# Optimization experiments

Measured on AMD Instinct MI355X. Metric: run time of the kernel, lower is better.

The kernel has to match this reference:

```python
import jax, jax.numpy as jnp
import numpy as np

TAU = 2.0      # LIF membrane time constant (spikingjelly LIFNode tau=2.0)
V_TH = 1.0     # default spikingjelly threshold
ALPHA = 2.0    # ATan surrogate default alpha

@jax.custom_vjp
def atan_spike(x):
    # Heaviside forward, ATan surrogate backward (spikingjelly surrogate.ATan)
    return (x >= 0.0).astype(x.dtype)

def _spike_fwd(x):
    return atan_spike(x), x

def _spike_bwd(x, g):
    sg = (ALPHA / 2.0) / (1.0 + (jnp.pi / 2.0 * ALPHA * x) ** 2)
    return (g * sg,)

atan_spike.defvjp(_spike_fwd, _spike_bwd)


def setup_inputs() -> dict:
    key = jax.random.key(0)
    ks = jax.random.split(key, 4)
    B, L, C, H, NL, K = 64, 96, 32, 256, 2, 3
    inputs = jax.random.normal(ks[0], (B, L, C), jnp.float32)
    w_enc = jax.random.normal(ks[1], (H, 1, K), jnp.float32) * (1.0 / np.sqrt(K))
    b_enc = jnp.zeros((H,), jnp.float32)
    w_rnn = jax.random.normal(ks[2], (NL, H, H), jnp.float32) * (1.0 / np.sqrt(H))
    b_rnn = jnp.zeros((NL, H), jnp.float32)
    return {"inputs": inputs, "w_enc": w_enc, "b_enc": b_enc,
            "w_rnn": w_rnn, "b_rnn": b_rnn}


def reference(inputs, w_enc, b_enc, w_rnn, b_rnn):
    B, L, C = inputs.shape
    H = w_enc.shape[0]
    NL = w_rnn.shape[0]
    # --- 'conv' spike encoder: per-channel temporal conv -> [B*C, H, L] ---
    x = inputs.transpose(0, 2, 1).reshape(B * C, 1, L)
    h = jax.lax.conv_general_dilated(x, w_enc, (1,), 'SAME',
                                     dimension_numbers=('NCH', 'OIH', 'NCH'))
    h = h + b_enc[None, :, None]
    h = h.transpose(2, 0, 1)  # [L, B*C, H] time-major for scan

    def step(v, x_t):
        s = x_t
        new_v = []
        for l in range(NL):  # fixed small layer loop
            cur = s @ w_rnn[l].T + b_rnn[l]            # Linear
            vl = v[l] + (cur - v[l]) / TAU             # leaky integrate
            s = atan_spike(vl - V_TH)                  # fire (surrogate grad)
            vl = vl * (1.0 - jax.lax.stop_gradient(s)) # hard reset, detach_reset
            new_v.append(vl)
        return tuple(new_v), (s, new_v[-1])

    v0 = tuple(jnp.zeros((B * C, H), inputs.dtype) for _ in range(NL))
    _, (spks, mems) = jax.lax.scan(step, v0, h)
    # spks: [L, B*C, H] -> [B, C*H, L]
    spks = spks.reshape(L, B, C * H).transpose(1, 2, 0)
    return spks.transpose(0, 2, 1), spks[:, :, -1]
```

## Files before the change

kernel.cpp:

```cpp
#include <hip/hip_runtime.h>
#include <hip/hip_bf16.h>
#include <stdint.h>


using floatx4 = __attribute__((ext_vector_type(4))) float;
using intx4   = __attribute__((ext_vector_type(4))) int;

__global__ void prep_kernel(const float* __restrict__ w_enc,
                            const float* __restrict__ b_enc,
                            const float* __restrict__ w_rnn,
                            const float* __restrict__ b_rnn,
                            double* __restrict__ Wd,
                            double* __restrict__ C0d,
                            signed char* __restrict__ Bw8)
{
    const int o = blockIdx.x;
    const int lane = threadIdx.x;
    const float4 w0v = *(const float4*)(w_rnn + (size_t)o * 256 + lane * 4);
    double a0 = 0.0, a1 = 0.0, a2 = 0.0, ab = 0.0;
#pragma unroll
    for (int e = 0; e < 4; ++e) {
        const int i = lane * 4 + e;
        const double wv = (double)(((const float*)&w0v)[e]);
        a0 += wv * (double)w_enc[i * 3 + 0];
        a1 += wv * (double)w_enc[i * 3 + 1];
        a2 += wv * (double)w_enc[i * 3 + 2];
        ab += wv * (double)b_enc[i];
    }
    for (int off = 32; off > 0; off >>= 1) {
        a0 += __shfl_down(a0, off, 64);
        a1 += __shfl_down(a1, off, 64);
        a2 += __shfl_down(a2, off, 64);
        ab += __shfl_down(ab, off, 64);
    }
    if (lane == 0) {
        Wd[o * 3 + 0] = a0;
        Wd[o * 3 + 1] = a1;
        Wd[o * 3 + 2] = a2;
        C0d[o] = ab + (double)b_rnn[o];
    }
    const float4 w1v = *(const float4*)(w_rnn + 65536 + (size_t)o * 256 + lane * 4);
    unsigned int pack[4] = {0u, 0u, 0u, 0u};
#pragma unroll
    for (int e = 0; e < 4; ++e) {
        float f = ((const float*)&w1v)[e];
        int q = __double2int_rn((double)f * 134217728.0);
        int d3 = ((q + 64) & 127) - 64;  q = (q - d3) >> 7;
        int d2 = ((q + 64) & 127) - 64;  q = (q - d2) >> 7;
        int d1 = ((q + 64) & 127) - 64;  q = (q - d1) >> 7;
        int d0 = q;
        pack[0] |= ((unsigned int)(d0 & 0xFF)) << (8 * e);
        pack[1] |= ((unsigned int)(d1 & 0xFF)) << (8 * e);
        pack[2] |= ((unsigned int)(d2 & 0xFF)) << (8 * e);
        pack[3] |= ((unsigned int)(d3 & 0xFF)) << (8 * e);
    }
#pragma unroll
    for (int l = 0; l < 4; ++l)
        *(unsigned int*)(Bw8 + ((size_t)o * 4 + l) * 256 + lane * 4) = pack[l];
}

__global__ void enc_kernel(const float* __restrict__ inputs,
                           const double* __restrict__ Wd,
                           const double* __restrict__ C0d,
                           unsigned char* __restrict__ s0b)
{
    const int n = blockIdx.x;
    const int tidx = threadIdx.x;
    const int b = n >> 5, c = n & 31;
    __shared__ float xr[98];
    if (tidx < 96)       xr[tidx + 1] = inputs[((size_t)b * 96 + tidx) * 32 + c];
    else if (tidx == 96) xr[0]  = 0.0f;
    else if (tidx == 97) xr[97] = 0.0f;
    __syncthreads();
    const double W0 = Wd[tidx * 3], W1 = Wd[tidx * 3 + 1], W2 = Wd[tidx * 3 + 2];
    const double c0 = C0d[tidx];
    const int wid = tidx >> 6, lane = tidx & 63;
    float v = 0.0f;
    for (int t = 0; t < 96; ++t) {
        float cur = (float)((double)xr[t] * W0 + (double)xr[t + 1] * W1 +
                            (double)xr[t + 2] * W2 + c0);
        float vv = v + (cur - v) * 0.5f;
        int sp = (vv - 1.0f) >= 0.0f;
        v = sp ? 0.0f : vv;
        unsigned long long bal = __ballot(sp);
        if ((lane & 15) == 0) {
            const int j = lane >> 4;
            *(unsigned short*)(s0b + ((size_t)t * 2048 + n) * 32 + 8 * j + 2 * wid)
                = (unsigned short)(bal >> (16 * j));
        }
    }
}

__global__ __launch_bounds__(256, 2) void rnn_kernel(
    const unsigned char* __restrict__ s0b,
    const signed char* __restrict__ Bw8,
    const float* __restrict__ b_rnn,
    float* __restrict__ out0,
    float* __restrict__ out1)
{
    const int tid  = threadIdx.x;
    const int wid  = tid >> 6, lane = tid & 63;
    const int m    = lane & 15, g = lane >> 4;
    const int job  = blockIdx.x * 4 + wid;
    const int rt   = job >> 4;
    const int nw   = rt * 16;
    const int o0   = (job & 15) * 16;

    intx4 bfrag[4][4];
#pragma unroll
    for (int l = 0; l < 4; ++l)
#pragma unroll
        for (int c = 0; c < 4; ++c)
            bfrag[l][c] = *(const intx4*)(Bw8 + ((size_t)(o0 + m) * 4 + l) * 256
                                               + c * 64 + g * 16);
    const float4 biasv = *(const float4*)(b_rnn + 256 + o0 + g * 4);

    float* pb = out0 + ((size_t)(nw >> 5) * 96) * 8192
                     + (size_t)((nw & 31) + m) * 256 + o0 + g * 4;

    const unsigned char* mp = s0b + ((size_t)(nw + m)) * 32 + 8 * g;
    uint2 m0 = *(const uint2*)(mp);
    uint2 m1 = *(const uint2*)(mp + 65536);

    floatx4 v = {0.f, 0.f, 0.f, 0.f};

    #define STEP_MFMA(MASK, ACC0, ACC1, ACC2, ACC3)                            \
    do {                                                                       \
        unsigned int hw_[4] = { (MASK).x & 0xFFFFu, (MASK).x >> 16,            \
                                (MASK).y & 0xFFFFu, (MASK).y >> 16 };          \
        _Pragma("unroll")                                                      \
        for (int c = 0; c < 4; ++c) {                                          \
            unsigned int h_ = hw_[c];                                          \
            intx4 a_;                                                          \
            a_.x = (int)((( h_        & 0xFu) * 0x00204081u) & 0x01010101u);   \
            a_.y = (int)((((h_ >> 4)  & 0xFu) * 0x00204081u) & 0x01010101u);   \
            a_.z = (int)((((h_ >> 8)  & 0xFu) * 0x00204081u) & 0x01010101u);   \
            a_.w = (int)((((h_ >> 12) & 0xFu) * 0x00204081u) & 0x01010101u);   \
            ACC0 = __builtin_amdgcn_mfma_i32_16x16x64_i8(bfrag[0][c], a_, ACC0, 0, 0, 0); \
            ACC1 = __builtin_amdgcn_mfma_i32_16x16x64_i8(bfrag[1][c], a_, ACC1, 0, 0, 0); \
            ACC2 = __builtin_amdgcn_mfma_i32_16x16x64_i8(bfrag[2][c], a_, ACC2, 0, 0, 0); \
            ACC3 = __builtin_amdgcn_mfma_i32_16x16x64_i8(bfrag[3][c], a_, ACC3, 0, 0, 0); \
        }                                                                      \
    } while (0)

    for (int t = 0; t < 95; ++t) {
        uint2 nxt = m1;
        m1 = *(const uint2*)(mp + (size_t)(t + 2) * 65536);

        intx4 acc0 = {0,0,0,0}, acc1 = {0,0,0,0}, acc2 = {0,0,0,0}, acc3 = {0,0,0,0};
        STEP_MFMA(m0, acc0, acc1, acc2, acc3);

        float4 sv;
#pragma unroll
        for (int r = 0; r < 4; ++r) {
            int a01 = acc0[r] * 128 + acc1[r];
            int a23 = acc2[r] * 128 + acc3[r];
            float cur = fmaf((float)a01, 0x1p-13f, (float)a23 * 0x1p-27f)
                        + ((const float*)&biasv)[r];
            float vv = v[r];
            vv = vv + (cur - vv) * 0.5f;
            float s = ((vv - 1.0f) >= 0.0f) ? 1.0f : 0.0f;
            v[r] = vv * (1.0f - s);
            ((float*)&sv)[r] = s;
        }
        *(float4*)pb = sv;
        pb += 8192;
        m0 = nxt;
    }

    {
        intx4 acc0 = {0,0,0,0}, acc1 = {0,0,0,0}, acc2 = {0,0,0,0}, acc3 = {0,0,0,0};
        STEP_MFMA(m0, acc0, acc1, acc2, acc3);
        float4 sv;
#pragma unroll
        for (int r = 0; r < 4; ++r) {
            int a01 = acc0[r] * 128 + acc1[r];
            int a23 = acc2[r] * 128 + acc3[r];
            float cur = fmaf((float)a01, 0x1p-13f, (float)a23 * 0x1p-27f)
                        + ((const float*)&biasv)[r];
            float vv = v[r];
            vv = vv + (cur - vv) * 0.5f;
            float s = ((vv - 1.0f) >= 0.0f) ? 1.0f : 0.0f;
            ((float*)&sv)[r] = s;
        }
        *(float4*)pb = sv;
        *(float4*)(out1 + (size_t)(nw + m) * 256 + o0 + g * 4) = sv;
    }
    #undef STEP_MFMA
}

extern "C" void kernel_launch(void* const* d_in, const int* in_sizes, int n_in,
                              void* d_out, int out_size, void* d_ws, size_t ws_size,
                              hipStream_t stream) {
    const float* inputs = (const float*)d_in[0];
    const float* w_enc  = (const float*)d_in[1];
    const float* b_enc  = (const float*)d_in[2];
    const float* w_rnn  = (const float*)d_in[3];
    const float* b_rnn  = (const float*)d_in[4];

    float* out0 = (float*)d_out;
    float* out1 = out0 + (size_t)64 * 96 * 8192;

    char* ws = (char*)d_ws;
    double*      Wd  = (double*)(ws);
    double*      C0d = (double*)(ws + 6144);
    signed char* Bw8 = (signed char*)(ws + 8192);
    unsigned char* s0b = (unsigned char*)(ws + 270336);

    prep_kernel<<<256, 64, 0, stream>>>(w_enc, b_enc, w_rnn, b_rnn, Wd, C0d, Bw8);
    enc_kernel<<<2048, 256, 0, stream>>>(inputs, Wd, C0d, s0b);
    rnn_kernel<<<512, 256, 0, stream>>>(s0b, Bw8, b_rnn, out0, out1);
}
```

Measured before the change: 257.9 us.

## Store layer-0 spikes as bytes to skip bitmask expansion in RNN kernel

The encoder now writes each layer-0 spike as a full byte instead of a ballot-packed bitmask. The RNN kernel then loads the bytes directly as int8 MFMA A-fragments, removing the per-step multiply-and-mask bit expansion. The cost is an 8x larger intermediate buffer (about 48 MB instead of 6 MB), which raises global memory write and read traffic and uses more workspace. The spike/reset select is also rewritten from multiply form to select form.

```diff
diff --git a/kernel.cpp b/kernel.cpp
--- a/kernel.cpp
+++ b/kernel.cpp
@@ -62,7 +62,7 @@
 __global__ void enc_kernel(const float* __restrict__ inputs,
                            const double* __restrict__ Wd,
                            const double* __restrict__ C0d,
-                           unsigned char* __restrict__ s0b)
+                           unsigned char* __restrict__ s0B)
 {
     const int n = blockIdx.x;
     const int tidx = threadIdx.x;
@@ -74,7 +74,7 @@
     __syncthreads();
     const double W0 = Wd[tidx * 3], W1 = Wd[tidx * 3 + 1], W2 = Wd[tidx * 3 + 2];
     const double c0 = C0d[tidx];
-    const int wid = tidx >> 6, lane = tidx & 63;
+    unsigned char* po = s0B + (size_t)n * 256 + tidx;
     float v = 0.0f;
     for (int t = 0; t < 96; ++t) {
         float cur = (float)((double)xr[t] * W0 + (double)xr[t + 1] * W1 +
@@ -82,17 +82,12 @@
         float vv = v + (cur - v) * 0.5f;
         int sp = (vv - 1.0f) >= 0.0f;
         v = sp ? 0.0f : vv;
-        unsigned long long bal = __ballot(sp);
-        if ((lane & 15) == 0) {
-            const int j = lane >> 4;
-            *(unsigned short*)(s0b + ((size_t)t * 2048 + n) * 32 + 8 * j + 2 * wid)
-                = (unsigned short)(bal >> (16 * j));
-        }
+        po[(size_t)t * 524288] = (unsigned char)sp;
     }
 }
 
 __global__ __launch_bounds__(256, 2) void rnn_kernel(
-    const unsigned char* __restrict__ s0b,
+    const unsigned char* __restrict__ s0B,
     const signed char* __restrict__ Bw8,
     const float* __restrict__ b_rnn,
     float* __restrict__ out0,
@@ -118,37 +113,45 @@
     float* pb = out0 + ((size_t)(nw >> 5) * 96) * 8192
                      + (size_t)((nw & 31) + m) * 256 + o0 + g * 4;
 
-    const unsigned char* mp = s0b + ((size_t)(nw + m)) * 32 + 8 * g;
-    uint2 m0 = *(const uint2*)(mp);
-    uint2 m1 = *(const uint2*)(mp + 65536);
+    const unsigned char* sp_base = s0B + (size_t)(nw + m) * 256 + 16 * g;
+    uint4 cb0 = *(const uint4*)(sp_base);
+    uint4 cb1 = *(const uint4*)(sp_base + 64);
+    uint4 cb2 = *(const uint4*)(sp_base + 128);
+    uint4 cb3 = *(const uint4*)(sp_base + 192);
 
     floatx4 v = {0.f, 0.f, 0.f, 0.f};
 
-    #define STEP_MFMA(MASK, ACC0, ACC1, ACC2, ACC3)                            \
+    #define STEP_MFMA(B0, B1, B2, B3, ACC0, ACC1, ACC2, ACC3)                  \
     do {                                                                       \
-        unsigned int hw_[4] = { (MASK).x & 0xFFFFu, (MASK).x >> 16,            \
-                                (MASK).y & 0xFFFFu, (MASK).y >> 16 };          \
-        _Pragma("unroll")                                                      \
-        for (int c = 0; c < 4; ++c) {                                          \
-            unsigned int h_ = hw_[c];                                          \
-            intx4 a_;                                                          \
-            a_.x = (int)((( h_        & 0xFu) * 0x00204081u) & 0x01010101u);   \
-            a_.y = (int)((((h_ >> 4)  & 0xFu) * 0x00204081u) & 0x01010101u);   \
-            a_.z = (int)((((h_ >> 8)  & 0xFu) * 0x00204081u) & 0x01010101u);   \
-            a_.w = (int)((((h_ >> 12) & 0xFu) * 0x00204081u) & 0x01010101u);   \
-            ACC0 = __builtin_amdgcn_mfma_i32_16x16x64_i8(bfrag[0][c], a_, ACC0, 0, 0, 0); \
-            ACC1 = __builtin_amdgcn_mfma_i32_16x16x64_i8(bfrag[1][c], a_, ACC1, 0, 0, 0); \
-            ACC2 = __builtin_amdgcn_mfma_i32_16x16x64_i8(bfrag[2][c], a_, ACC2, 0, 0, 0); \
-            ACC3 = __builtin_amdgcn_mfma_i32_16x16x64_i8(bfrag[3][c], a_, ACC3, 0, 0, 0); \
-        }                                                                      \
+        intx4 a0_ = *(intx4*)&(B0), a1_ = *(intx4*)&(B1),                      \
+              a2_ = *(intx4*)&(B2), a3_ = *(intx4*)&(B3);                      \
+        ACC0 = __builtin_amdgcn_mfma_i32_16x16x64_i8(bfrag[0][0], a0_, ACC0, 0, 0, 0); \
+        ACC1 = __builtin_amdgcn_mfma_i32_16x16x64_i8(bfrag[1][0], a0_, ACC1, 0, 0, 0); \
+        ACC2 = __builtin_amdgcn_mfma_i32_16x16x64_i8(bfrag[2][0], a0_, ACC2, 0, 0, 0); \
+        ACC3 = __builtin_amdgcn_mfma_i32_16x16x64_i8(bfrag[3][0], a0_, ACC3, 0, 0, 0); \
+        ACC0 = __builtin_amdgcn_mfma_i32_16x16x64_i8(bfrag[0][1], a1_, ACC0, 0, 0, 0); \
+        ACC1 = __builtin_amdgcn_mfma_i32_16x16x64_i8(bfrag[1][1], a1_, ACC1, 0, 0, 0); \
+        ACC2 = __builtin_amdgcn_mfma_i32_16x16x64_i8(bfrag[2][1], a1_, ACC2, 0, 0, 0); \
+        ACC3 = __builtin_amdgcn_mfma_i32_16x16x64_i8(bfrag[3][1], a1_, ACC3, 0, 0, 0); \
+        ACC0 = __builtin_amdgcn_mfma_i32_16x16x64_i8(bfrag[0][2], a2_, ACC0, 0, 0, 0); \
+        ACC1 = __builtin_amdgcn_mfma_i32_16x16x64_i8(bfrag[1][2], a2_, ACC1, 0, 0, 0); \
+        ACC2 = __builtin_amdgcn_mfma_i32_16x16x64_i8(bfrag[2][2], a2_, ACC2, 0, 0, 0); \
+        ACC3 = __builtin_amdgcn_mfma_i32_16x16x64_i8(bfrag[3][2], a2_, ACC3, 0, 0, 0); \
+        ACC0 = __builtin_amdgcn_mfma_i32_16x16x64_i8(bfrag[0][3], a3_, ACC0, 0, 0, 0); \
+        ACC1 = __builtin_amdgcn_mfma_i32_16x16x64_i8(bfrag[1][3], a3_, ACC1, 0, 0, 0); \
+        ACC2 = __builtin_amdgcn_mfma_i32_16x16x64_i8(bfrag[2][3], a3_, ACC2, 0, 0, 0); \
+        ACC3 = __builtin_amdgcn_mfma_i32_16x16x64_i8(bfrag[3][3], a3_, ACC3, 0, 0, 0); \
     } while (0)
 
     for (int t = 0; t < 95; ++t) {
-        uint2 nxt = m1;
-        m1 = *(const uint2*)(mp + (size_t)(t + 2) * 65536);
+        const unsigned char* q = sp_base + (size_t)(t + 1) * 524288;
+        uint4 nb0 = *(const uint4*)(q);
+        uint4 nb1 = *(const uint4*)(q + 64);
+        uint4 nb2 = *(const uint4*)(q + 128);
+        uint4 nb3 = *(const uint4*)(q + 192);
 
         intx4 acc0 = {0,0,0,0}, acc1 = {0,0,0,0}, acc2 = {0,0,0,0}, acc3 = {0,0,0,0};
-        STEP_MFMA(m0, acc0, acc1, acc2, acc3);
+        STEP_MFMA(cb0, cb1, cb2, cb3, acc0, acc1, acc2, acc3);
 
         float4 sv;
 #pragma unroll
@@ -159,18 +162,18 @@
                         + ((const float*)&biasv)[r];
             float vv = v[r];
             vv = vv + (cur - vv) * 0.5f;
-            float s = ((vv - 1.0f) >= 0.0f) ? 1.0f : 0.0f;
-            v[r] = vv * (1.0f - s);
-            ((float*)&sv)[r] = s;
+            bool sp = (vv - 1.0f) >= 0.0f;
+            v[r] = sp ? 0.0f : vv;
+            ((float*)&sv)[r] = sp ? 1.0f : 0.0f;
         }
         *(float4*)pb = sv;
         pb += 8192;
-        m0 = nxt;
+        cb0 = nb0; cb1 = nb1; cb2 = nb2; cb3 = nb3;
     }
 
     {
         intx4 acc0 = {0,0,0,0}, acc1 = {0,0,0,0}, acc2 = {0,0,0,0}, acc3 = {0,0,0,0};
-        STEP_MFMA(m0, acc0, acc1, acc2, acc3);
+        STEP_MFMA(cb0, cb1, cb2, cb3, acc0, acc1, acc2, acc3);
         float4 sv;
 #pragma unroll
         for (int r = 0; r < 4; ++r) {
@@ -180,8 +183,8 @@
                         + ((const float*)&biasv)[r];
             float vv = v[r];
             vv = vv + (cur - vv) * 0.5f;
-            float s = ((vv - 1.0f) >= 0.0f) ? 1.0f : 0.0f;
-            ((float*)&sv)[r] = s;
+            bool sp = (vv - 1.0f) >= 0.0f;
+            ((float*)&sv)[r] = sp ? 1.0f : 0.0f;
         }
         *(float4*)pb = sv;
         *(float4*)(out1 + (size_t)(nw + m) * 256 + o0 + g * 4) = sv;
@@ -202,12 +205,12 @@
     float* out1 = out0 + (size_t)64 * 96 * 8192;
 
     char* ws = (char*)d_ws;
-    double*      Wd  = (double*)(ws);
-    double*      C0d = (double*)(ws + 6144);
-    signed char* Bw8 = (signed char*)(ws + 8192);
-    unsigned char* s0b = (unsigned char*)(ws + 270336);
+    double*        Wd  = (double*)(ws);
+    double*        C0d = (double*)(ws + 6144);
+    signed char*   Bw8 = (signed char*)(ws + 8192);
+    unsigned char* s0B = (unsigned char*)(ws + 270336);
 
     prep_kernel<<<256, 64, 0, stream>>>(w_enc, b_enc, w_rnn, b_rnn, Wd, C0d, Bw8);
-    enc_kernel<<<2048, 256, 0, stream>>>(inputs, Wd, C0d, s0b);
-    rnn_kernel<<<512, 256, 0, stream>>>(s0b, Bw8, b_rnn, out0, out1);
-}
+    enc_kernel<<<2048, 256, 0, stream>>>(inputs, Wd, C0d, s0B);
+    rnn_kernel<<<512, 256, 0, stream>>>(s0B, Bw8, b_rnn, out0, out1);
+}
```

Result: slower. 297.2 us (+15.2%).
